# Kernel optimization log

Hardware: AMD Instinct MI355X
Metric: run time of the kernel (lower is better)

The kernel has to match this reference:

```python
import jax, jax.numpy as jnp
import numpy as np

N, T, IN, H, OUT, E = 50000, 12, 2, 128, 12, 800000


def setup_inputs() -> dict:
    key = jax.random.key(0)
    ks = jax.random.split(key, 20)
    s_in = 1.0 / np.sqrt(H)

    def w(k, shape):
        return jax.random.uniform(k, shape, jnp.float32, -s_in, s_in)

    return {
        "x": jax.random.normal(ks[0], (N, T, IN), jnp.float32),
        "edge_index": jax.random.randint(ks[1], (2, E), 0, N, dtype=jnp.int32),
        # LSTM layer 0 (input_dim -> H), gate order i,f,g,o as in PyTorch
        "Wih0": w(ks[2], (4 * H, IN)), "Whh0": w(ks[3], (4 * H, H)),
        "bih0": w(ks[4], (4 * H,)), "bhh0": w(ks[5], (4 * H,)),
        # LSTM layer 1 (H -> H)
        "Wih1": w(ks[6], (4 * H, H)), "Whh1": w(ks[7], (4 * H, H)),
        "bih1": w(ks[8], (4 * H,)), "bhh1": w(ks[9], (4 * H,)),
        # GCN layers
        "W0": w(ks[10], (H, H)), "b0": w(ks[11], (H,)),
        "W1": w(ks[12], (H, H)), "b1": w(ks[13], (H,)),
        "W2": w(ks[14], (H, OUT)), "b2": w(ks[15], (OUT,)),
    }


def _lstm_layer(seq, Wih, Whh, bih, bhh):
    # seq: [T, N, D] -> outputs [T, N, H]
    n = seq.shape[1]
    h0 = jnp.zeros((n, H), seq.dtype)
    c0 = jnp.zeros((n, H), seq.dtype)
    b = bih + bhh

    def step(carry, xt):
        h, c = carry
        z = xt @ Wih.T + h @ Whh.T + b
        i, f, g, o = jnp.split(z, 4, axis=-1)
        c = jax.nn.sigmoid(f) * c + jax.nn.sigmoid(i) * jnp.tanh(g)
        h = jax.nn.sigmoid(o) * jnp.tanh(c)
        return (h, c), h

    _, ys = jax.lax.scan(step, (h0, c0), seq)
    return ys


def _gcn(h, W, b, src, dst, norm):
    # x @ W, gather sources, edge-normalize, scatter-add to targets, + bias
    hW = h @ W
    msg = hW[src] * norm[:, None]
    return jax.ops.segment_sum(msg, dst, num_segments=N) + b


def reference(x, edge_index, Wih0, Whh0, bih0, bhh0, Wih1, Whh1, bih1, bhh1,
              W0, b0, W1, b1, W2, b2):
    # 2-layer LSTM over node time series (dropout inactive at inference)
    seq = jnp.transpose(x, (1, 0, 2))          # [T, N, IN]
    y0 = _lstm_layer(seq, Wih0, Whh0, bih0, bhh0)
    y1 = _lstm_layer(y0, Wih1, Whh1, bih1, bhh1)
    h = y1[-1]                                  # last timestep: [N, H]

    # GCN normalization with self-loops (symmetric, all edge weights 1)
    loops = jnp.arange(N, dtype=edge_index.dtype)
    src = jnp.concatenate([edge_index[0], loops])
    dst = jnp.concatenate([edge_index[1], loops])
    deg = jax.ops.segment_sum(jnp.ones(src.shape[0], h.dtype), dst, num_segments=N)
    dinv = jax.lax.rsqrt(deg)                   # deg >= 1 thanks to self-loops
    norm = dinv[src] * dinv[dst]

    h = jax.nn.relu(_gcn(h, W0, b0, src, dst, norm))
    h = jax.nn.relu(_gcn(h, W1, b1, src, dst, norm))
    out = _gcn(h, W2, b2, src, dst, norm)       # [N, OUT]
    return out
```

## Files before the change

kernel.cpp:

```cpp
#include <hip/hip_runtime.h>
#include <hip/hip_bf16.h>

#define TT 12
#define HDIM 128
#define ODIM 12
#define KS0 136
#define TPAD 36

typedef short bf16x8 __attribute__((ext_vector_type(8)));
typedef float f32x16 __attribute__((ext_vector_type(16)));
typedef float f32x4  __attribute__((ext_vector_type(4)));

__device__ __forceinline__ float fastrcp(float x) { return __builtin_amdgcn_rcpf(x); }
__device__ __forceinline__ float sigf(float x) { return fastrcp(1.f + __expf(-x)); }
__device__ __forceinline__ float tanh_fast(float x) { return 1.f - 2.f * fastrcp(1.f + __expf(2.f * x)); }
__device__ __forceinline__ unsigned short f2bf(float f) {
    union { float f; unsigned int u; } v; v.f = f;
    unsigned int r = v.u + 0x7FFFu + ((v.u >> 16) & 1u);
    return (unsigned short)(r >> 16);
}

__global__ void pack_kernel(const float* __restrict__ Whh0, const float* __restrict__ Wih1,
                            const float* __restrict__ Whh1, unsigned short* __restrict__ Wpk)
{
    int idx = blockIdx.x * 256 + threadIdx.x;
    if (idx >= 384 * 64) return;
    int lane = idx & 63;
    int slot = idx >> 6;
    int mat = slot >> 7;
    int rem = slot & 127;
    if (mat == 0) {
        int cb = rem >> 3, s = rem & 7;
        int col = cb * 32 + (lane & 31);
#pragma unroll
        for (int j = 0; j < 8; ++j) {
            int k = s * 16 + ((lane >> 5) << 3) + j;
            Wpk[((size_t)(slot * 64 + lane) << 3) + j] = f2bf(Whh0[col * 128 + k]);
        }
    } else {
        const float* src = (mat == 1) ? Wih1 : Whh1;
        int ct = rem >> 2, ks = rem & 3;
        int col = ct * 16 + (lane & 15);
#pragma unroll
        for (int j = 0; j < 8; ++j) {
            int k = ks * 32 + ((lane >> 4) << 3) + j;
            Wpk[((size_t)(slot * 64 + lane) << 3) + j] = f2bf(src[col * 128 + k]);
        }
    }
}

__global__ __launch_bounds__(512, 1) void lstm_l0_kernel(
    const float* __restrict__ x,
    const unsigned short* __restrict__ Wpk,
    const float* __restrict__ Wih0,
    const float* __restrict__ bih0, const float* __restrict__ bhh0,
    unsigned short* __restrict__ h0seq,
    int N, int ntiles)
{
    __shared__ unsigned short wlds[65536];
    __shared__ unsigned short hA0[64 * KS0];
    __shared__ float xls[64 * 24];

    const int tid  = threadIdx.x;
    const int w    = tid >> 6;
    const int ln   = tid & 63;
    const int ln31 = ln & 31;
    const int half = ln >> 5;
    const int wsub = w & 3;
    const int rb   = w >> 2;
    const int col  = wsub * 32 + ln31;
    const int cm   = tid >> 3;
    const int cc0  = (tid & 7) << 4;

    for (int i = tid * 8; i < 65536; i += 512 * 8)
        *(bf16x8*)(wlds + i) = *(const bf16x8*)(Wpk + i);

    float wx0[4], wx1[4], br0[4];
#pragma unroll
    for (int g = 0; g < 4; ++g) {
        int row = (g << 7) + col;
        wx0[g] = Wih0[row * 2 + 0];
        wx1[g] = Wih0[row * 2 + 1];
        br0[g] = bih0[row] + bhh0[row];
    }

    for (int tile = blockIdx.x; tile < ntiles; tile += gridDim.x) {
        const int nbase = tile * 64;
        __syncthreads();
        for (int i = tid; i < 64 * 24; i += 512) {
            int n = nbase + i / 24;
            xls[i] = (n < N) ? x[nbase * 24 + i] : 0.f;
        }
        for (int i = tid; i < 64 * KS0; i += 512) hA0[i] = 0;
        float c0[16];
#pragma unroll
        for (int r = 0; r < 16; ++r) c0[r] = 0.f;
        __syncthreads();

        const int ncp = nbase + cm;
        const bool cok = ncp < N;

        for (int t = 0; t < TT; ++t) {
            f32x16 acc[4];
#pragma unroll
            for (int g = 0; g < 4; ++g)
#pragma unroll
                for (int e = 0; e < 16; ++e) acc[g][e] = 0.f;
#pragma unroll
            for (int s = 0; s < 8; ++s) {
                bf16x8 a = *(const bf16x8*)(hA0 + (rb * 32 + ln31) * KS0 + s * 16 + half * 8);
#pragma unroll
                for (int g = 0; g < 4; ++g) {
                    int cb = g * 4 + wsub;
                    bf16x8 b = *(const bf16x8*)(wlds + (((cb * 8 + s) * 64 + ln) << 3));
                    acc[g] = __builtin_amdgcn_mfma_f32_32x32x16_bf16(a, b, acc[g], 0, 0, 0);
                }
            }
            __syncthreads();
#pragma unroll
            for (int r = 0; r < 16; ++r) {
                int node = rb * 32 + (r & 3) + 8 * (r >> 2) + 4 * half;
                float xa = xls[node * 24 + t * 2 + 0];
                float xb = xls[node * 24 + t * 2 + 1];
                float zi = acc[0][r] + br0[0] + wx0[0] * xa + wx1[0] * xb;
                float zf = acc[1][r] + br0[1] + wx0[1] * xa + wx1[1] * xb;
                float zg = acc[2][r] + br0[2] + wx0[2] * xa + wx1[2] * xb;
                float zo = acc[3][r] + br0[3] + wx0[3] * xa + wx1[3] * xb;
                float cn = sigf(zf) * c0[r] + sigf(zi) * tanh_fast(zg);
                c0[r] = cn;
                float h = sigf(zo) * tanh_fast(cn);
                hA0[node * KS0 + col] = f2bf(h);
            }
            __syncthreads();
            if (cok) {
                bf16x8 v0 = *(const bf16x8*)(hA0 + cm * KS0 + cc0);
                bf16x8 v1 = *(const bf16x8*)(hA0 + cm * KS0 + cc0 + 8);
                unsigned short* dp = h0seq + ((size_t)ncp * TT + t) * HDIM + cc0;
                *(bf16x8*)(dp)     = v0;
                *(bf16x8*)(dp + 8) = v1;
            }
        }
    }
}

__global__ __launch_bounds__(512) void lstm_l1f_kernel(
    const unsigned short* __restrict__ h0seq,
    const unsigned short* __restrict__ Wpk,
    const float* __restrict__ bih1, const float* __restrict__ bhh1,
    float* __restrict__ hbuf,
    int N, int ntiles)
{
    __shared__ unsigned short wlds[65536];
    __shared__ unsigned short hA1[2][8192];

    const int tid  = threadIdx.x;
    const int w    = tid >> 6;
    const int ln   = tid & 63;
    const int l15  = ln & 15;
    const int quad = ln >> 4;
    const int ch   = w * 16 + l15;
    const int chk  = ch >> 5;
    const int chq  = (ch >> 3) & 3;
    const int chj  = ch & 7;

    for (int i = tid * 8; i < 65536; i += 512 * 8)
        *(bf16x8*)(wlds + i) = *(const bf16x8*)(Wpk + 131072 + i);

    bf16x8 wfr[4][4];
#pragma unroll
    for (int g = 0; g < 4; ++g)
#pragma unroll
        for (int ks = 0; ks < 4; ++ks) {
            int slot = (g * 8 + w) * 4 + ks;
            wfr[g][ks] = *(const bf16x8*)(Wpk + 65536 + ((size_t)(slot * 64 + ln) << 3));
        }

    float br1[4];
#pragma unroll
    for (int g = 0; g < 4; ++g) {
        int row = (g << 7) + ch;
        br1[g] = bih1[row] + bhh1[row];
    }

    const bf16x8 zv = {0, 0, 0, 0, 0, 0, 0, 0};
    __syncthreads();

    for (int tile = blockIdx.x; tile < ntiles; tile += gridDim.x) {
        __syncthreads();
        for (int i = tid; i < 1024; i += 512)
            *(bf16x8*)(hA1[0] + i * 8) = zv;
        float c1[16];
#pragma unroll
        for (int r = 0; r < 16; ++r) c1[r] = 0.f;

        int na[4]; bool ok[4];
#pragma unroll
        for (int rt = 0; rt < 4; ++rt) { na[rt] = tile * 64 + rt * 16 + l15; ok[rt] = na[rt] < N; }
        __syncthreads();

        for (int t = 0; t < TT; ++t) {
            const unsigned short* usp = hA1[t & 1];
            unsigned short* dst = hA1[(t & 1) ^ 1];

            f32x4 acc[4][4];
#pragma unroll
            for (int rt = 0; rt < 4; ++rt)
#pragma unroll
                for (int g = 0; g < 4; ++g)
#pragma unroll
                    for (int e = 0; e < 4; ++e) acc[rt][g][e] = 0.f;

#pragma unroll
            for (int ks = 0; ks < 4; ++ks) {
                bf16x8 a[4];
#pragma unroll
                for (int rt = 0; rt < 4; ++rt)
                    a[rt] = ok[rt]
                        ? *(const bf16x8*)(h0seq + ((size_t)na[rt] * TT + t) * HDIM + ks * 32 + quad * 8)
                        : zv;
#pragma unroll
                for (int g = 0; g < 4; ++g)
#pragma unroll
                    for (int rt = 0; rt < 4; ++rt)
                        acc[rt][g] = __builtin_amdgcn_mfma_f32_16x16x32_bf16(a[rt], wfr[g][ks], acc[rt][g], 0, 0, 0);
            }
#pragma unroll
            for (int ks = 0; ks < 4; ++ks) {
                bf16x8 a[4];
#pragma unroll
                for (int rt = 0; rt < 4; ++rt)
                    a[rt] = *(const bf16x8*)(usp + (((rt * 4 + ks) * 64 + ln) << 3));
#pragma unroll
                for (int g = 0; g < 4; ++g) {
                    int slot = (g * 8 + w) * 4 + ks;
                    bf16x8 b = *(const bf16x8*)(wlds + ((size_t)(slot * 64 + ln) << 3));
#pragma unroll
                    for (int rt = 0; rt < 4; ++rt)
                        acc[rt][g] = __builtin_amdgcn_mfma_f32_16x16x32_bf16(a[rt], b, acc[rt][g], 0, 0, 0);
                }
            }

#pragma unroll
            for (int rt = 0; rt < 4; ++rt) {
#pragma unroll
                for (int rg = 0; rg < 4; ++rg) {
                    int ci = rt * 4 + rg;
                    float zi = acc[rt][0][rg] + br1[0];
                    float zf = acc[rt][1][rg] + br1[1];
                    float zg = acc[rt][2][rg] + br1[2];
                    float zo = acc[rt][3][rg] + br1[3];
                    float cn = sigf(zf) * c1[ci] + sigf(zi) * tanh_fast(zg);
                    c1[ci] = cn;
                    float h = sigf(zo) * tanh_fast(cn);
                    if (t + 1 < TT) {
                        dst[(((rt * 4 + chk) * 64 + chq * 16 + quad * 4 + rg) << 3) + chj] = f2bf(h);
                    } else {
                        int n = tile * 64 + rt * 16 + quad * 4 + rg;
                        if (n < N) hbuf[n * HDIM + ch] = h;
                    }
                }
            }
            __syncthreads();
        }
    }
}

__global__ void deg_count_kernel(const int* __restrict__ ei, int* __restrict__ degi, int E)
{
    int e = blockIdx.x * 256 + threadIdx.x;
    if (e < E) atomicAdd(&degi[ei[E + e]], 1);
}

__global__ void row_alloc_kernel(const int* __restrict__ degi, int* __restrict__ row_ptr,
                                 float* __restrict__ dinv, int* __restrict__ counter, int N)
{
    int n = blockIdx.x * 256 + threadIdx.x;
    int lane = threadIdx.x & 63;
    int v = (n < N) ? degi[n] : 0;
    int incl = v;
    for (int off = 1; off < 64; off <<= 1) {
        int u = __shfl_up(incl, off);
        if (lane >= off) incl += u;
    }
    int base = 0;
    if (lane == 63) base = atomicAdd(counter, incl);
    base = __shfl(base, 63);
    if (n < N) {
        row_ptr[n] = base + (incl - v);
        dinv[n] = rsqrtf((float)(v + 1));
    }
}

__global__ void csr_fill_kernel(const int* __restrict__ ei, const int* __restrict__ row_ptr,
                                int* __restrict__ fill, int* __restrict__ csr_src, int E)
{
    int e = blockIdx.x * 256 + threadIdx.x;
    if (e < E) {
        int d = ei[E + e];
        int p = atomicAdd(&fill[d], 1);
        csr_src[row_ptr[d] + p] = ei[e];
    }
}

__global__ __launch_bounds__(256) void gemm128_kernel(const float* __restrict__ X,
                                                      const float* __restrict__ W,
                                                      _Float16* __restrict__ Y, int N)
{
    __shared__ float XT[128 * TPAD];
    const int tid = threadIdx.x;
    const int nbase = blockIdx.x * 32;
    for (int idx = tid; idx < 32 * 128; idx += 256) {
        int m = idx >> 7, k = idx & 127;
        int n = nbase + m;
        XT[k * TPAD + m] = (n < N) ? X[n * HDIM + k] : 0.f;
    }
    __syncthreads();
    const int c  = tid & 63;
    const int mb = (tid >> 6) << 3;
    float acc[8][2];
#pragma unroll
    for (int i = 0; i < 8; ++i) { acc[i][0] = 0.f; acc[i][1] = 0.f; }
    for (int k = 0; k < 128; ++k) {
        const float* xr = &XT[k * TPAD + mb];
        float4 a0 = *(const float4*)(xr);
        float4 a1 = *(const float4*)(xr + 4);
        float a[8] = {a0.x, a0.y, a0.z, a0.w, a1.x, a1.y, a1.z, a1.w};
        float b0 = W[k * HDIM + c];
        float b1 = W[k * HDIM + c + 64];
#pragma unroll
        for (int i = 0; i < 8; ++i) {
            acc[i][0] = fmaf(a[i], b0, acc[i][0]);
            acc[i][1] = fmaf(a[i], b1, acc[i][1]);
        }
    }
#pragma unroll
    for (int i = 0; i < 8; ++i) {
        int n = nbase + mb + i;
        if (n < N) {
            Y[n * HDIM + c]      = (_Float16)acc[i][0];
            Y[n * HDIM + c + 64] = (_Float16)acc[i][1];
        }
    }
}

__global__ void gemm12_kernel(const float* __restrict__ X, const float* __restrict__ W2,
                              _Float16* __restrict__ Y, int N)
{
    int idx = blockIdx.x * 256 + threadIdx.x;
    int n = idx / ODIM, c = idx - n * ODIM;
    if (n >= N) return;
    float acc = 0.f;
    for (int k = 0; k < 128; ++k) acc = fmaf(X[n * HDIM + k], W2[k * ODIM + c], acc);
    Y[n * ODIM + c] = (_Float16)acc;
}

__global__ __launch_bounds__(128) void agg128_kernel(const _Float16* __restrict__ hW,
        const int* __restrict__ row_ptr, const int* __restrict__ degi,
        const int* __restrict__ csr_src, const float* __restrict__ dinv,
        const float* __restrict__ bias, float* __restrict__ out, int N, int do_relu)
{
    int n = blockIdx.x;
    int c = threadIdx.x;
    float dn = dinv[n];
    float acc = (float)hW[n * HDIM + c] * dn * dn;
    int start = row_ptr[n];
    int cnt = degi[n];
    for (int i = 0; i < cnt; ++i) {
        int s = csr_src[start + i];
        acc = fmaf((float)hW[s * HDIM + c], dinv[s] * dn, acc);
    }
    float v = acc + bias[c];
    if (do_relu) v = fmaxf(v, 0.f);
    out[n * HDIM + c] = v;
}

__global__ void agg12_kernel(const _Float16* __restrict__ hW, const int* __restrict__ row_ptr,
        const int* __restrict__ degi, const int* __restrict__ csr_src,
        const float* __restrict__ dinv, const float* __restrict__ b2,
        float* __restrict__ out, int N)
{
    int idx = blockIdx.x * 256 + threadIdx.x;
    int n = idx / ODIM, c = idx - n * ODIM;
    if (n >= N) return;
    float dn = dinv[n];
    float acc = (float)hW[n * ODIM + c] * dn * dn;
    int start = row_ptr[n], cnt = degi[n];
    for (int i = 0; i < cnt; ++i) {
        int s = csr_src[start + i];
        acc = fmaf((float)hW[s * ODIM + c], dinv[s] * dn, acc);
    }
    out[n * ODIM + c] = acc + b2[c];
}

extern "C" void kernel_launch(void* const* d_in, const int* in_sizes, int n_in,
                              void* d_out, int out_size, void* d_ws, size_t ws_size,
                              hipStream_t stream)
{
    const float* x     = (const float*)d_in[0];
    const int*   ei    = (const int*)d_in[1];
    const float* Wih0  = (const float*)d_in[2];
    const float* Whh0  = (const float*)d_in[3];
    const float* bih0  = (const float*)d_in[4];
    const float* bhh0  = (const float*)d_in[5];
    const float* Wih1  = (const float*)d_in[6];
    const float* Whh1  = (const float*)d_in[7];
    const float* bih1  = (const float*)d_in[8];
    const float* bhh1  = (const float*)d_in[9];
    const float* W0    = (const float*)d_in[10];
    const float* b0    = (const float*)d_in[11];
    const float* W1    = (const float*)d_in[12];
    const float* b1    = (const float*)d_in[13];
    const float* W2    = (const float*)d_in[14];
    const float* b2    = (const float*)d_in[15];
    float* out = (float*)d_out;

    const int N = in_sizes[0] / (TT * 2);
    const int E = in_sizes[1] / 2;

    unsigned short* Wpk = (unsigned short*)d_ws;
    float* fbase = (float*)((char*)d_ws + 393216);
    float* hbuf = fbase;
    float* buf1 = hbuf + (size_t)N * HDIM;
    float* buf2 = buf1 + (size_t)N * HDIM;
    float* dinv = buf2 + (size_t)N * HDIM;
    int* degi    = (int*)(dinv + N);
    int* fill    = degi + N;
    int* counter = fill + N;
    int* row_ptr = counter + 1;
    int* csr_src = row_ptr + N;
    size_t h0_off = (((size_t)((char*)(csr_src + E) - (char*)d_ws)) + 255) & ~(size_t)255;
    unsigned short* h0seq = (unsigned short*)((char*)d_ws + h0_off);
    _Float16* buf1h = (_Float16*)buf1;

    hipMemsetAsync(degi, 0, (size_t)(2 * N + 1) * sizeof(int), stream);

    pack_kernel<<<(384 * 64 + 255) / 256, 256, 0, stream>>>(Whh0, Wih1, Whh1, Wpk);

    const int ntiles = (N + 63) / 64;
    lstm_l0_kernel<<<256, 512, 0, stream>>>(x, Wpk, Wih0, bih0, bhh0, h0seq, N, ntiles);
    lstm_l1f_kernel<<<256, 512, 0, stream>>>(h0seq, Wpk, bih1, bhh1, hbuf, N, ntiles);

    deg_count_kernel<<<(E + 255) / 256, 256, 0, stream>>>(ei, degi, E);
    row_alloc_kernel<<<(N + 255) / 256, 256, 0, stream>>>(degi, row_ptr, dinv, counter, N);
    csr_fill_kernel<<<(E + 255) / 256, 256, 0, stream>>>(ei, row_ptr, fill, csr_src, E);

    gemm128_kernel<<<(N + 31) / 32, 256, 0, stream>>>(hbuf, W0, buf1h, N);
    agg128_kernel<<<N, 128, 0, stream>>>(buf1h, row_ptr, degi, csr_src, dinv, b0, buf2, N, 1);
    gemm128_kernel<<<(N + 31) / 32, 256, 0, stream>>>(buf2, W1, buf1h, N);
    agg128_kernel<<<N, 128, 0, stream>>>(buf1h, row_ptr, degi, csr_src, dinv, b1, buf2, N, 1);
    gemm12_kernel<<<((size_t)N * ODIM + 255) / 256, 256, 0, stream>>>(buf2, W2, buf1h, N);
    agg12_kernel<<<((size_t)N * ODIM + 255) / 256, 256, 0, stream>>>(
        buf1h, row_ptr, degi, csr_src, dinv, b2, out, N);
}
```

Baseline: 1.037 ms.

## Store layer-0 LSTM outputs in MFMA fragment order per tile and timestep

Layer 0 now writes its hidden states into a tile-major buffer whose order matches the A-operand fragments that layer 1's MFMA consumes. Layer 1 can then load each fragment with one contiguous, coalesced 16-byte read per lane and no bounds checks, instead of strided per-node gathers. The layer-1 K loop is also restructured so the h0 loads and the recurrent-state loads are issued together, interleaving the two MFMA chains. The buffer now always holds full padded tiles, which adds a little extra workspace for the tail tile.

Result: faster. 940.2 us (-9.3%).

```diff
diff --git a/kernel.cpp b/kernel.cpp
--- a/kernel.cpp
+++ b/kernel.cpp
@@ -54,7 +54,7 @@
     const unsigned short* __restrict__ Wpk,
     const float* __restrict__ Wih0,
     const float* __restrict__ bih0, const float* __restrict__ bhh0,
-    unsigned short* __restrict__ h0seq,
+    unsigned short* __restrict__ h0f,
     int N, int ntiles)
 {
     __shared__ unsigned short wlds[65536];
@@ -69,8 +69,6 @@
     const int wsub = w & 3;
     const int rb   = w >> 2;
     const int col  = wsub * 32 + ln31;
-    const int cm   = tid >> 3;
-    const int cc0  = (tid & 7) << 4;
 
     for (int i = tid * 8; i < 65536; i += 512 * 8)
         *(bf16x8*)(wlds + i) = *(const bf16x8*)(Wpk + i);
@@ -96,9 +94,6 @@
 #pragma unroll
         for (int r = 0; r < 16; ++r) c0[r] = 0.f;
         __syncthreads();
-
-        const int ncp = nbase + cm;
-        const bool cok = ncp < N;
 
         for (int t = 0; t < TT; ++t) {
             f32x16 acc[4];
@@ -132,19 +127,25 @@
                 hA0[node * KS0 + col] = f2bf(h);
             }
             __syncthreads();
-            if (cok) {
-                bf16x8 v0 = *(const bf16x8*)(hA0 + cm * KS0 + cc0);
-                bf16x8 v1 = *(const bf16x8*)(hA0 + cm * KS0 + cc0 + 8);
-                unsigned short* dp = h0seq + ((size_t)ncp * TT + t) * HDIM + cc0;
-                *(bf16x8*)(dp)     = v0;
-                *(bf16x8*)(dp + 8) = v1;
+            {
+                unsigned short* dt = h0f + (((size_t)(tile * TT + t)) << 13);
+#pragma unroll
+                for (int it = 0; it < 2; ++it) {
+                    int i = tid + it * 512;
+                    int rtks = i >> 6;
+                    int lane = i & 63;
+                    int m   = ((rtks >> 2) << 4) + (lane & 15);
+                    int chb = ((rtks & 3) << 5) + ((lane >> 4) << 3);
+                    bf16x8 v = *(const bf16x8*)(hA0 + m * KS0 + chb);
+                    *(bf16x8*)(dt + ((size_t)i << 3)) = v;
+                }
             }
         }
     }
 }
 
 __global__ __launch_bounds__(512) void lstm_l1f_kernel(
-    const unsigned short* __restrict__ h0seq,
+    const unsigned short* __restrict__ h0f,
     const unsigned short* __restrict__ Wpk,
     const float* __restrict__ bih1, const float* __restrict__ bhh1,
     float* __restrict__ hbuf,
@@ -192,15 +193,12 @@
         float c1[16];
 #pragma unroll
         for (int r = 0; r < 16; ++r) c1[r] = 0.f;
-
-        int na[4]; bool ok[4];
-#pragma unroll
-        for (int rt = 0; rt < 4; ++rt) { na[rt] = tile * 64 + rt * 16 + l15; ok[rt] = na[rt] < N; }
         __syncthreads();
 
         for (int t = 0; t < TT; ++t) {
             const unsigned short* usp = hA1[t & 1];
             unsigned short* dst = hA1[(t & 1) ^ 1];
+            const unsigned short* h0t = h0f + (((size_t)(tile * TT + t)) << 13);
 
             f32x4 acc[4][4];
 #pragma unroll
@@ -212,32 +210,27 @@
 
 #pragma unroll
             for (int ks = 0; ks < 4; ++ks) {
-                bf16x8 a[4];
+                bf16x8 a0[4];
 #pragma unroll
                 for (int rt = 0; rt < 4; ++rt)
-                    a[rt] = ok[rt]
-                        ? *(const bf16x8*)(h0seq + ((size_t)na[rt] * TT + t) * HDIM + ks * 32 + quad * 8)
-                        : zv;
-#pragma unroll
-                for (int g = 0; g < 4; ++g)
-#pragma unroll
-                    for (int rt = 0; rt < 4; ++rt)
-                        acc[rt][g] = __builtin_amdgcn_mfma_f32_16x16x32_bf16(a[rt], wfr[g][ks], acc[rt][g], 0, 0, 0);
-            }
-#pragma unroll
-            for (int ks = 0; ks < 4; ++ks) {
-                bf16x8 a[4];
+                    a0[rt] = *(const bf16x8*)(h0t + (((rt * 4 + ks) * 64 + ln) << 3));
+                bf16x8 a1[4];
 #pragma unroll
                 for (int rt = 0; rt < 4; ++rt)
-                    a[rt] = *(const bf16x8*)(usp + (((rt * 4 + ks) * 64 + ln) << 3));
+                    a1[rt] = *(const bf16x8*)(usp + (((rt * 4 + ks) * 64 + ln) << 3));
 #pragma unroll
                 for (int g = 0; g < 4; ++g) {
                     int slot = (g * 8 + w) * 4 + ks;
                     bf16x8 b = *(const bf16x8*)(wlds + ((size_t)(slot * 64 + ln) << 3));
 #pragma unroll
                     for (int rt = 0; rt < 4; ++rt)
-                        acc[rt][g] = __builtin_amdgcn_mfma_f32_16x16x32_bf16(a[rt], b, acc[rt][g], 0, 0, 0);
+                        acc[rt][g] = __builtin_amdgcn_mfma_f32_16x16x32_bf16(a1[rt], b, acc[rt][g], 0, 0, 0);
                 }
+#pragma unroll
+                for (int g = 0; g < 4; ++g)
+#pragma unroll
+                    for (int rt = 0; rt < 4; ++rt)
+                        acc[rt][g] = __builtin_amdgcn_mfma_f32_16x16x32_bf16(a0[rt], wfr[g][ks], acc[rt][g], 0, 0, 0);
             }
 
 #pragma unroll
@@ -416,6 +409,7 @@
 
     const int N = in_sizes[0] / (TT * 2);
     const int E = in_sizes[1] / 2;
+    const int ntiles = (N + 63) / 64;
 
     unsigned short* Wpk = (unsigned short*)d_ws;
     float* fbase = (float*)((char*)d_ws + 393216);
@@ -429,16 +423,15 @@
     int* row_ptr = counter + 1;
     int* csr_src = row_ptr + N;
     size_t h0_off = (((size_t)((char*)(csr_src + E) - (char*)d_ws)) + 255) & ~(size_t)255;
-    unsigned short* h0seq = (unsigned short*)((char*)d_ws + h0_off);
+    unsigned short* h0f = (unsigned short*)((char*)d_ws + h0_off);
     _Float16* buf1h = (_Float16*)buf1;
 
     hipMemsetAsync(degi, 0, (size_t)(2 * N + 1) * sizeof(int), stream);
 
     pack_kernel<<<(384 * 64 + 255) / 256, 256, 0, stream>>>(Whh0, Wih1, Whh1, Wpk);
 
-    const int ntiles = (N + 63) / 64;
-    lstm_l0_kernel<<<256, 512, 0, stream>>>(x, Wpk, Wih0, bih0, bhh0, h0seq, N, ntiles);
-    lstm_l1f_kernel<<<256, 512, 0, stream>>>(h0seq, Wpk, bih1, bhh1, hbuf, N, ntiles);
+    lstm_l0_kernel<<<256, 512, 0, stream>>>(x, Wpk, Wih0, bih0, bhh0, h0f, N, ntiles);
+    lstm_l1f_kernel<<<256, 512, 0, stream>>>(h0f, Wpk, bih1, bhh1, hbuf, N, ntiles);
 
     deg_count_kernel<<<(E + 255) / 256, 256, 0, stream>>>(ei, degi, E);
     row_alloc_kernel<<<(N + 255) / 256, 256, 0, stream>>>(degi, row_ptr, dinv, counter, N);
```
